# Kernel tuning notes

Measured on AMD Instinct MI355X. Metric: run time of the kernel, lower is better.

## Reference

```python
import jax, jax.numpy as jnp
import numpy as np

# Model dims (match init_kwargs)
B_, L, D_MODEL = 1, 2048, 1024
D_INNER, D_CONV, DT_RANK, D_STATE = 2048, 4, 64, 16


def setup_inputs() -> dict:
    key = jax.random.key(0)
    ks = jax.random.split(key, 8)
    s = lambda k, shape, scale: jax.random.normal(k, shape, jnp.float32) * scale
    return {
        "x": jax.random.normal(ks[0], (B_, L, D_MODEL), jnp.float32),
        "in_proj_w": s(ks[1], (D_MODEL, 2 * D_INNER), 0.02),
        "in_proj_b": jnp.zeros((2 * D_INNER,), jnp.float32),
        "conv_w": s(ks[2], (D_CONV, D_INNER), 0.1),          # depthwise kernel, one tap-vector per channel
        "conv_b": jnp.zeros((D_INNER,), jnp.float32),
        "x_proj_w": s(ks[3], (D_INNER, DT_RANK + 2 * D_STATE), 0.02),
        "dt_proj_w": s(ks[4], (DT_RANK, D_INNER), 0.1),
        "dt_proj_b": s(ks[5], (D_INNER,), 0.1),
        "A_log": jnp.log(jnp.tile(jnp.arange(1, D_STATE + 1, dtype=jnp.float32), (D_INNER, 1))),  # S4D-real init
        "D": jnp.ones((D_INNER,), jnp.float32),
        "out_proj_w": s(ks[6], (D_INNER, D_MODEL), 0.02),
        "out_proj_b": jnp.zeros((D_MODEL,), jnp.float32),
    }


def _mamba_forward(x, in_proj_w, in_proj_b, conv_w, conv_b, x_proj_w,
                   dt_proj_w, dt_proj_b, A_log, D, out_proj_w, out_proj_b):
    b, l, _ = x.shape
    d_inner = conv_w.shape[1]
    d_state = A_log.shape[1]

    # in_proj -> split into ssm path and gating residual
    x_and_res = x @ in_proj_w + in_proj_b                 # [b, l, 2*d_inner]
    xin, res = jnp.split(x_and_res, 2, axis=-1)

    # causal depthwise conv1d over the sequence dim (pad left d_conv-1, trunc to l)
    xp = jnp.pad(xin, ((0, 0), (D_CONV - 1, 0), (0, 0)))
    kern = conv_w[:, None, :]                             # [W, I=1, O=d_inner]
    xc = jax.lax.conv_general_dilated(
        xp, kern, window_strides=(1,), padding="VALID",
        dimension_numbers=("NWC", "WIO", "NWC"),
        feature_group_count=d_inner) + conv_b             # [b, l, d_inner]
    u = jax.nn.silu(xc)

    # selective SSM: input-dependent dt, B, C
    A = -jnp.exp(A_log)                                   # [d_inner, d_state]
    dbc = u @ x_proj_w                                    # [b, l, dt_rank + 2*d_state]
    dt, Bm, Cm = jnp.split(dbc, [DT_RANK, DT_RANK + d_state], axis=-1)
    delta = jax.nn.softplus(dt @ dt_proj_w + dt_proj_b)   # [b, l, d_inner]

    deltaA = jnp.exp(jnp.einsum("bld,dn->bldn", delta, A))          # [b, l, d_inner, d_state]
    deltaBu = jnp.einsum("bld,bln,bld->bldn", delta, Bm, u)         # [b, l, d_inner, d_state]

    def step(h, inp):
        dA_t, dBu_t, C_t = inp
        h = dA_t * h + dBu_t                              # [b, d_inner, d_state]
        y_t = jnp.einsum("bdn,bn->bd", h, C_t)
        return h, y_t

    h0 = jnp.zeros((b, d_inner, d_state), u.dtype)
    _, ys = jax.lax.scan(
        step, h0,
        (deltaA.transpose(1, 0, 2, 3), deltaBu.transpose(1, 0, 2, 3), Cm.transpose(1, 0, 2)))
    y = ys.transpose(1, 0, 2) + u * D                     # skip connection via D

    # gate and out-project
    y = y * jax.nn.silu(res)
    return y @ out_proj_w + out_proj_b                    # [b, l, d_model]


def reference(x, in_proj_w, in_proj_b, conv_w, conv_b, x_proj_w,
              dt_proj_w, dt_proj_b, A_log, D, out_proj_w, out_proj_b):
    return _mamba_forward(x, in_proj_w, in_proj_b, conv_w, conv_b, x_proj_w,
                          dt_proj_w, dt_proj_b, A_log, D, out_proj_w, out_proj_b)
```

## Files before the change

### kernel.cpp

```cpp
#include <hip/hip_runtime.h>


#define L_SEQ 2048
#define DMODEL 1024
#define DINNER 2048
#define NSTATE 16
#define DTRANK 64
#define NPROJ_PAD 128
#define NCH 128
#define TCH 16

typedef __attribute__((ext_vector_type(8))) short short8;
typedef __attribute__((ext_vector_type(4))) float f32x4;

__device__ __forceinline__ unsigned short f2bf(float f) {
  unsigned int u = __float_as_uint(f);
  u += 0x7FFFu + ((u >> 16) & 1u);
  return (unsigned short)(u >> 16);
}
__device__ __forceinline__ float bf2f(unsigned short u) {
  return __uint_as_float(((unsigned int)u) << 16);
}

__device__ __forceinline__ void gload16(const void* g, void* l) {
  __builtin_amdgcn_global_load_lds((const __attribute__((address_space(1))) void*)g,
                                   (__attribute__((address_space(3))) void*)l, 16, 0, 0);
}

__global__ void prep_kernel(const float* __restrict__ in_proj_w, const float* __restrict__ x_proj_w,
                            const float* __restrict__ dt_proj_w,
                            const float* __restrict__ out_proj_w, const float* __restrict__ x,
                            unsigned short* __restrict__ w1t, unsigned short* __restrict__ w3t,
                            unsigned short* __restrict__ w4t, unsigned short* __restrict__ w5t,
                            unsigned short* __restrict__ xb) {
  const int bx = blockIdx.x;
  const int tx = threadIdx.x, ty = threadIdx.y;
  const int id = ty * 32 + tx;

  if (bx >= 6464) {
    if (bx < 8512) {
      const int fid = (bx - 6464) * 256 + id;
      f32x4 v = ((const f32x4*)x)[fid];
      ushort4 o;
      o.x = f2bf(v.x); o.y = f2bf(v.y); o.z = f2bf(v.z); o.w = f2bf(v.w);
      ((ushort4*)xb)[fid] = o;
    } else {
      const int fid = (bx - 8512) * 256 + id;
      ((uint4*)(w3t + 96 * 2048))[fid] = (uint4){0, 0, 0, 0};
    }
    return;
  }

  const float* in;
  unsigned short* out;
  int R, C, rel, gx;
  if (bx < 4096) { in = in_proj_w; out = w1t; R = 1024; C = 4096; rel = bx; gx = 128; }
  else if (bx < 4288) { in = x_proj_w; out = w3t; R = 2048; C = 96; rel = bx - 4096; gx = 3; }
  else if (bx < 4416) { in = dt_proj_w; out = w4t; R = 64; C = 2048; rel = bx - 4288; gx = 64; }
  else { in = out_proj_w; out = w5t; R = 2048; C = 1024; rel = bx - 4416; gx = 32; }
  const int c0 = (rel % gx) * 32, r0 = (rel / gx) * 32;

  __shared__ float tile[32][33];
  for (int y = ty; y < 32; y += 8) tile[y][tx] = in[(size_t)(r0 + y) * C + c0 + tx];
  __syncthreads();
  for (int y = ty; y < 32; y += 8) out[(size_t)(c0 + y) * R + r0 + tx] = f2bf(tile[tx][y]);
}

__global__ void conv_silu_kernel(const float* __restrict__ xin, const float* __restrict__ cw,
                                 const float* __restrict__ cb, unsigned short* __restrict__ ub) {
  const int id = blockIdx.x * 256 + threadIdx.x;
  const int t = id >> 11;
  const int d = id & (DINNER - 1);
  float acc = cb[d];
#pragma unroll
  for (int j = 0; j < 4; j++) {
    int tt = t - 3 + j;
    if (tt >= 0) acc += xin[(size_t)tt * DINNER + d] * cw[j * DINNER + d];
  }
  float s = acc / (1.f + __expf(-acc));
  ub[id] = f2bf(s);
}

template <int EPI, int BM, int BN>
__global__ void gemm_bf16(const unsigned short* __restrict__ A,
                          const unsigned short* __restrict__ Bt, float* __restrict__ C,
                          unsigned short* __restrict__ C2, const float* __restrict__ bias, int M,
                          int N, int K, int KS) {
  constexpr int MI = BM / 32, NJ = BN / 32;
  __shared__ __align__(16) unsigned short lA[2][BM * 64];
  __shared__ __align__(16) unsigned short lB[2][BN * 64];
  const int tid = threadIdx.x;
  const int w = tid >> 6;
  const int lane = tid & 63;
  const int m0 = blockIdx.x * BM;
  const int n0 = blockIdx.y * BN;
  const int kbase = blockIdx.z * KS;
  const int lr = lane >> 3;
  const int srcoff = ((lane & 7) ^ lr) * 8;
  const int wm = (w & 1) * (BM / 2);
  const int wn = (w >> 1) * (BN / 2);
  const int ml = lane & 15;
  const int quad = lane >> 4;

  f32x4 acc[MI][NJ];
#pragma unroll
  for (int i = 0; i < MI; i++)
#pragma unroll
    for (int j = 0; j < NJ; j++) acc[i][j] = (f32x4){0.f, 0.f, 0.f, 0.f};

  const unsigned short* Ag = A + (size_t)m0 * K + kbase;
  const unsigned short* Bg = Bt + (size_t)n0 * K + kbase;

  const int niter = KS >> 6;
  auto stage = [&](int buf, int kk) {
#pragma unroll
    for (int c2 = 0; c2 < BM / 32; c2++) {
      const int row = w * (BM / 4) + c2 * 8 + lr;
      gload16(Ag + (size_t)row * K + kk + srcoff, &lA[buf][(w * (BM / 4) + c2 * 8) * 64]);
    }
#pragma unroll
    for (int c2 = 0; c2 < BN / 32; c2++) {
      const int row = w * (BN / 4) + c2 * 8 + lr;
      gload16(Bg + (size_t)row * K + kk + srcoff, &lB[buf][(w * (BN / 4) + c2 * 8) * 64]);
    }
  };

  stage(0, 0);
  for (int it = 0; it < niter; it++) {
    __syncthreads();
    if (it + 1 < niter) stage((it + 1) & 1, (it + 1) << 6);
    const unsigned short* bufA = lA[it & 1];
    const unsigned short* bufB = lB[it & 1];
#pragma unroll
    for (int ks = 0; ks < 2; ks++) {
      short8 af[MI], bfr[NJ];
#pragma unroll
      for (int i = 0; i < MI; i++) {
        const int row = wm + i * 16 + ml;
        af[i] = *(const short8*)&bufA[row * 64 + ((ks * 4 + quad) ^ (ml & 7)) * 8];
      }
#pragma unroll
      for (int j = 0; j < NJ; j++) {
        const int row = wn + j * 16 + ml;
        bfr[j] = *(const short8*)&bufB[row * 64 + ((ks * 4 + quad) ^ (ml & 7)) * 8];
      }
#pragma unroll
      for (int i = 0; i < MI; i++)
#pragma unroll
        for (int j = 0; j < NJ; j++)
          acc[i][j] = __builtin_amdgcn_mfma_f32_16x16x32_bf16(af[i], bfr[j], acc[i][j], 0, 0, 0);
    }
  }

  float* Cp = (EPI == 3) ? C + (size_t)blockIdx.z * M * N : C;
#pragma unroll
  for (int i = 0; i < MI; i++) {
#pragma unroll
    for (int j = 0; j < NJ; j++) {
      const int col = n0 + wn + j * 16 + ml;
      float bv = (EPI == 3) ? 0.f : (bias ? bias[col] : 0.f);
#pragma unroll
      for (int r = 0; r < 4; r++) {
        const int row = m0 + wm + i * 16 + quad * 4 + r;
        float v = acc[i][j][r] + bv;
        if (EPI == 0) {
          Cp[(size_t)row * N + col] = v;
        } else if (EPI == 3) {
          Cp[(size_t)row * N + col] = v;
        } else if (EPI == 4) {
          if (col < DINNER) {
            C[(size_t)row * DINNER + col] = v;
          } else {
            float s = v / (1.f + __expf(-v));
            C2[(size_t)row * DINNER + (col - DINNER)] = f2bf(s);
          }
        } else if (EPI == 5) {
          float sp = (v > 15.f) ? v : __logf(1.f + __expf(v));
          C2[(size_t)row * N + col] = f2bf(sp);
        }
      }
    }
  }
}

__global__ void reduce_dbc_kernel(const float* __restrict__ part, float* __restrict__ dbc,
                                  unsigned short* __restrict__ dtb) {
  const int id = blockIdx.x * 256 + threadIdx.x;
  float s = 0.f;
#pragma unroll
  for (int z = 0; z < 8; z++) s += part[(size_t)z * (L_SEQ * NPROJ_PAD) + id];
  dbc[id] = s;
  const int col = id & 127;
  if (col < 64) dtb[(id >> 7) * 64 + col] = f2bf(s);
}


__global__ void scan1_kernel(const unsigned short* __restrict__ db,
                             const unsigned short* __restrict__ ub,
                             const float* __restrict__ dbc, const float* __restrict__ A_log,
                             unsigned short* __restrict__ P, unsigned short* __restrict__ Hz) {
  __shared__ float Bs[TCH][NSTATE];
  const int d = blockIdx.x * 256 + threadIdx.x;
  const int c = blockIdx.y;
  for (int idx = threadIdx.x; idx < TCH * NSTATE; idx += 256) {
    int t = idx >> 4, n = idx & 15;
    Bs[t][n] = dbc[(size_t)(c * TCH + t) * NPROJ_PAD + DTRANK + n];
  }
  float Ad[16], h[16], p[16];
#pragma unroll
  for (int n = 0; n < 16; n++) {
    Ad[n] = -__expf(A_log[d * 16 + n]);
    h[n] = 0.f;
    p[n] = 1.f;
  }
  __syncthreads();
#pragma unroll
  for (int t = 0; t < TCH; t++) {
    const int tt = c * TCH + t;
    float dl = bf2f(db[(size_t)tt * DINNER + d]);
    float uu = bf2f(ub[(size_t)tt * DINNER + d]);
    float du = dl * uu;
#pragma unroll
    for (int n = 0; n < 16; n++) {
      float dA = __expf(dl * Ad[n]);
      p[n] *= dA;
      h[n] = dA * h[n] + du * Bs[t][n];
    }
  }
#pragma unroll
  for (int n = 0; n < 16; n++) {
    P[(size_t)(c * 16 + n) * DINNER + d] = f2bf(p[n]);
    Hz[(size_t)(c * 16 + n) * DINNER + d] = f2bf(h[n]);
  }
}

__global__ void scan_carry_kernel(const unsigned short* __restrict__ P,
                                  const unsigned short* __restrict__ Hz,
                                  unsigned short* __restrict__ H0) {
  const int id = blockIdx.x * 256 + threadIdx.x;
  float h = 0.f;
#pragma unroll 8
  for (int c = 0; c < NCH; c++) {
    H0[c * (NSTATE * DINNER) + id] = f2bf(h);
    h = bf2f(P[c * (NSTATE * DINNER) + id]) * h + bf2f(Hz[c * (NSTATE * DINNER) + id]);
  }
}

__global__ void scan2_kernel(const unsigned short* __restrict__ db,
                             const unsigned short* __restrict__ ub,
                             const float* __restrict__ dbc, const float* __restrict__ A_log,
                             const float* __restrict__ Dv, const unsigned short* __restrict__ rsil,
                             const unsigned short* __restrict__ H0,
                             unsigned short* __restrict__ ygb) {
  __shared__ float Bs[TCH][NSTATE];
  __shared__ float Cs[TCH][NSTATE];
  const int d = blockIdx.x * 256 + threadIdx.x;
  const int c = blockIdx.y;
  for (int idx = threadIdx.x; idx < TCH * 2 * NSTATE; idx += 256) {
    int t = idx >> 5, q = idx & 31;
    float v = dbc[(size_t)(c * TCH + t) * NPROJ_PAD + DTRANK + q];
    if (q < 16) Bs[t][q] = v;
    else Cs[t][q - 16] = v;
  }
  float Ad[16], h[16];
#pragma unroll
  for (int n = 0; n < 16; n++) {
    Ad[n] = -__expf(A_log[d * 16 + n]);
    h[n] = bf2f(H0[(size_t)(c * 16 + n) * DINNER + d]);
  }
  const float Dd = Dv[d];
  __syncthreads();
#pragma unroll
  for (int t = 0; t < TCH; t++) {
    const int tt = c * TCH + t;
    float dl = bf2f(db[(size_t)tt * DINNER + d]);
    float uu = bf2f(ub[(size_t)tt * DINNER + d]);
    float rs = bf2f(rsil[(size_t)tt * DINNER + d]);
    float du = dl * uu;
    float y0 = 0.f, y1 = 0.f;
#pragma unroll
    for (int n = 0; n < 16; n++) {
      float dA = __expf(dl * Ad[n]);
      h[n] = dA * h[n] + du * Bs[t][n];
      if (n & 1) y1 += h[n] * Cs[t][n];
      else y0 += h[n] * Cs[t][n];
    }
    float yg = (y0 + y1 + uu * Dd) * rs;
    ygb[(size_t)tt * DINNER + d] = f2bf(yg);
  }
}


extern "C" void kernel_launch(void* const* d_in, const int* in_sizes, int n_in, void* d_out,
                              int out_size, void* d_ws, size_t ws_size, hipStream_t stream) {
  const float* x = (const float*)d_in[0];
  const float* in_proj_w = (const float*)d_in[1];
  const float* in_proj_b = (const float*)d_in[2];
  const float* conv_w = (const float*)d_in[3];
  const float* conv_b = (const float*)d_in[4];
  const float* x_proj_w = (const float*)d_in[5];
  const float* dt_proj_w = (const float*)d_in[6];
  const float* dt_proj_b = (const float*)d_in[7];
  const float* A_log = (const float*)d_in[8];
  const float* Dvec = (const float*)d_in[9];
  const float* out_proj_w = (const float*)d_in[10];
  const float* out_proj_b = (const float*)d_in[11];
  float* out = (float*)d_out;
  char* ws = (char*)d_ws;
  (void)in_sizes; (void)n_in; (void)out_size; (void)ws_size;

  const size_t MB = 1048576;
  const size_t XB = 0;
  const size_t W1T = 4 * MB;
  const size_t XIN = 12 * MB;
  const size_t RSIL = 28 * MB;
  const size_t UB = 36 * MB;
  const size_t W3T = 44 * MB;
  const size_t DBC = W3T + 524288;
  const size_t DTB = DBC + MB;
  const size_t W4T = DTB + 262144;
  const size_t DELTA = 46 * MB;
  const size_t YGB = 54 * MB;
  const size_t W5T = 62 * MB;
  const size_t G3P = 66 * MB;
  const size_t PB = 74 * MB;
  const size_t HZB = 82 * MB;
  const size_t H0B = 90 * MB;

  prep_kernel<<<8544, dim3(32, 8), 0, stream>>>(
      in_proj_w, x_proj_w, dt_proj_w, out_proj_w, x, (unsigned short*)(ws + W1T),
      (unsigned short*)(ws + W3T), (unsigned short*)(ws + W4T), (unsigned short*)(ws + W5T),
      (unsigned short*)(ws + XB));

  gemm_bf16<4, 128, 128><<<dim3(16, 32, 1), 256, 0, stream>>>(
      (const unsigned short*)(ws + XB), (const unsigned short*)(ws + W1T), (float*)(ws + XIN),
      (unsigned short*)(ws + RSIL), in_proj_b, 2048, 4096, 1024, 1024);

  conv_silu_kernel<<<(L_SEQ * DINNER) / 256, 256, 0, stream>>>(
      (const float*)(ws + XIN), conv_w, conv_b, (unsigned short*)(ws + UB));

  gemm_bf16<3, 64, 128><<<dim3(32, 1, 8), 256, 0, stream>>>(
      (const unsigned short*)(ws + UB), (const unsigned short*)(ws + W3T), (float*)(ws + G3P),
      nullptr, nullptr, 2048, NPROJ_PAD, 2048, 256);
  reduce_dbc_kernel<<<(L_SEQ * NPROJ_PAD) / 256, 256, 0, stream>>>(
      (const float*)(ws + G3P), (float*)(ws + DBC), (unsigned short*)(ws + DTB));

  gemm_bf16<5, 128, 128><<<dim3(16, 16, 1), 256, 0, stream>>>(
      (const unsigned short*)(ws + DTB), (const unsigned short*)(ws + W4T), nullptr,
      (unsigned short*)(ws + DELTA), dt_proj_b, 2048, 2048, 64, 64);

  const dim3 sgrid(DINNER / 256, NCH);
  scan1_kernel<<<sgrid, 256, 0, stream>>>(
      (const unsigned short*)(ws + DELTA), (const unsigned short*)(ws + UB),
      (const float*)(ws + DBC), A_log, (unsigned short*)(ws + PB), (unsigned short*)(ws + HZB));
  scan_carry_kernel<<<(NSTATE * DINNER) / 256, 256, 0, stream>>>(
      (const unsigned short*)(ws + PB), (const unsigned short*)(ws + HZB),
      (unsigned short*)(ws + H0B));
  scan2_kernel<<<sgrid, 256, 0, stream>>>(
      (const unsigned short*)(ws + DELTA), (const unsigned short*)(ws + UB),
      (const float*)(ws + DBC), A_log, Dvec, (const unsigned short*)(ws + RSIL),
      (const unsigned short*)(ws + H0B), (unsigned short*)(ws + YGB));

  gemm_bf16<0, 64, 64><<<dim3(32, 16, 1), 256, 0, stream>>>(
      (const unsigned short*)(ws + YGB), (const unsigned short*)(ws + W5T), out, nullptr,
      out_proj_b, 2048, 1024, 2048, 2048);
}
```

Baseline: 230.5 us.

## Fuse chunked scan phases into cooperative kernel and store conv input as bf16

The three scan stages (per-chunk scan, carry propagation, final scan) become one cooperative kernel separated by grid-wide syncs, with a fallback to the old three launches if the cooperative launch fails. The in_proj epilogue now writes the conv input as bf16 instead of fp32, which halves that intermediate's write and read traffic. The conv+SiLU kernel now computes four timesteps per thread and reuses the overlapping loaded inputs. The aim is to cut launch overhead and memory traffic, at the cost of needing all 1024 blocks co-resident and slightly lower precision for the conv input.

After: 529.2 us. 130% more time.

```diff
diff --git a/kernel.cpp b/kernel.cpp
--- a/kernel.cpp
+++ b/kernel.cpp
@@ -1,4 +1,5 @@
 #include <hip/hip_runtime.h>
+#include <hip/hip_cooperative_groups.h>
 
 
 #define L_SEQ 2048
@@ -9,6 +10,8 @@
 #define NPROJ_PAD 128
 #define NCH 128
 #define TCH 16
+
+namespace cg = cooperative_groups;
 
 typedef __attribute__((ext_vector_type(8))) short short8;
 typedef __attribute__((ext_vector_type(4))) float f32x4;
@@ -66,19 +69,26 @@
   for (int y = ty; y < 32; y += 8) out[(size_t)(c0 + y) * R + r0 + tx] = f2bf(tile[tx][y]);
 }
 
-__global__ void conv_silu_kernel(const float* __restrict__ xin, const float* __restrict__ cw,
-                                 const float* __restrict__ cb, unsigned short* __restrict__ ub) {
+__global__ void conv_silu_kernel(const unsigned short* __restrict__ xin,
+                                 const float* __restrict__ cw, const float* __restrict__ cb,
+                                 unsigned short* __restrict__ ub) {
   const int id = blockIdx.x * 256 + threadIdx.x;
-  const int t = id >> 11;
   const int d = id & (DINNER - 1);
-  float acc = cb[d];
-#pragma unroll
-  for (int j = 0; j < 4; j++) {
-    int tt = t - 3 + j;
-    if (tt >= 0) acc += xin[(size_t)tt * DINNER + d] * cw[j * DINNER + d];
-  }
-  float s = acc / (1.f + __expf(-acc));
-  ub[id] = f2bf(s);
+  const int t0 = (id >> 11) * 4;
+  float xv[7];
+#pragma unroll
+  for (int j = 0; j < 7; j++) {
+    int tt = t0 - 3 + j;
+    xv[j] = (tt >= 0) ? bf2f(xin[(size_t)tt * DINNER + d]) : 0.f;
+  }
+  float w0 = cw[d], w1 = cw[DINNER + d], w2 = cw[2 * DINNER + d], w3 = cw[3 * DINNER + d];
+  const float b = cb[d];
+#pragma unroll
+  for (int k = 0; k < 4; k++) {
+    float acc = b + xv[k] * w0 + xv[k + 1] * w1 + xv[k + 2] * w2 + xv[k + 3] * w3;
+    float s = acc / (1.f + __expf(-acc));
+    ub[(size_t)(t0 + k) * DINNER + d] = f2bf(s);
+  }
 }
 
 template <int EPI, int BM, int BN>
@@ -163,13 +173,11 @@
       for (int r = 0; r < 4; r++) {
         const int row = m0 + wm + i * 16 + quad * 4 + r;
         float v = acc[i][j][r] + bv;
-        if (EPI == 0) {
-          Cp[(size_t)row * N + col] = v;
-        } else if (EPI == 3) {
+        if (EPI == 0 || EPI == 3) {
           Cp[(size_t)row * N + col] = v;
         } else if (EPI == 4) {
           if (col < DINNER) {
-            C[(size_t)row * DINNER + col] = v;
+            ((unsigned short*)C)[(size_t)row * DINNER + col] = f2bf(v);
           } else {
             float s = v / (1.f + __expf(-v));
             C2[(size_t)row * DINNER + (col - DINNER)] = f2bf(s);
@@ -195,17 +203,10 @@
 }
 
 
-__global__ void scan1_kernel(const unsigned short* __restrict__ db,
-                             const unsigned short* __restrict__ ub,
-                             const float* __restrict__ dbc, const float* __restrict__ A_log,
-                             unsigned short* __restrict__ P, unsigned short* __restrict__ Hz) {
-  __shared__ float Bs[TCH][NSTATE];
-  const int d = blockIdx.x * 256 + threadIdx.x;
-  const int c = blockIdx.y;
-  for (int idx = threadIdx.x; idx < TCH * NSTATE; idx += 256) {
-    int t = idx >> 4, n = idx & 15;
-    Bs[t][n] = dbc[(size_t)(c * TCH + t) * NPROJ_PAD + DTRANK + n];
-  }
+__device__ __forceinline__ void scan_phase1(const unsigned short* db, const unsigned short* ub,
+                                            const float* dbc, const float* A_log,
+                                            unsigned short* P, unsigned short* Hz, int d, int c,
+                                            float (&Bs)[TCH][NSTATE]) {
   float Ad[16], h[16], p[16];
 #pragma unroll
   for (int n = 0; n < 16; n++) {
@@ -232,6 +233,88 @@
     P[(size_t)(c * 16 + n) * DINNER + d] = f2bf(p[n]);
     Hz[(size_t)(c * 16 + n) * DINNER + d] = f2bf(h[n]);
   }
+}
+
+__device__ __forceinline__ void scan_phase3(const unsigned short* db, const unsigned short* ub,
+                                            const float* A_log, const float* Dv,
+                                            const unsigned short* rsil, const unsigned short* H0,
+                                            unsigned short* ygb, int d, int c,
+                                            float (&Bs)[TCH][NSTATE], float (&Cs)[TCH][NSTATE]) {
+  float Ad[16], h[16];
+#pragma unroll
+  for (int n = 0; n < 16; n++) {
+    Ad[n] = -__expf(A_log[d * 16 + n]);
+    h[n] = bf2f(H0[(size_t)(c * 16 + n) * DINNER + d]);
+  }
+  const float Dd = Dv[d];
+#pragma unroll
+  for (int t = 0; t < TCH; t++) {
+    const int tt = c * TCH + t;
+    float dl = bf2f(db[(size_t)tt * DINNER + d]);
+    float uu = bf2f(ub[(size_t)tt * DINNER + d]);
+    float rs = bf2f(rsil[(size_t)tt * DINNER + d]);
+    float du = dl * uu;
+    float y0 = 0.f, y1 = 0.f;
+#pragma unroll
+    for (int n = 0; n < 16; n++) {
+      float dA = __expf(dl * Ad[n]);
+      h[n] = dA * h[n] + du * Bs[t][n];
+      if (n & 1) y1 += h[n] * Cs[t][n];
+      else y0 += h[n] * Cs[t][n];
+    }
+    float yg = (y0 + y1 + uu * Dd) * rs;
+    ygb[(size_t)tt * DINNER + d] = f2bf(yg);
+  }
+}
+
+__device__ __forceinline__ void load_bc(const float* dbc, int c, float (&Bs)[TCH][NSTATE],
+                                        float (&Cs)[TCH][NSTATE], int tid) {
+  for (int idx = tid; idx < TCH * 2 * NSTATE; idx += 256) {
+    int t = idx >> 5, q = idx & 31;
+    float v = dbc[(size_t)(c * TCH + t) * NPROJ_PAD + DTRANK + q];
+    if (q < 16) Bs[t][q] = v;
+    else Cs[t][q - 16] = v;
+  }
+}
+
+__global__ void __launch_bounds__(256, 4)
+scan_fused_kernel(const unsigned short* __restrict__ db, const unsigned short* __restrict__ ub,
+                  const float* __restrict__ dbc, const float* __restrict__ A_log,
+                  const float* __restrict__ Dv, const unsigned short* __restrict__ rsil,
+                  unsigned short* __restrict__ P, unsigned short* __restrict__ Hz,
+                  unsigned short* __restrict__ H0, unsigned short* __restrict__ ygb) {
+  cg::grid_group grid = cg::this_grid();
+  __shared__ float Bs[TCH][NSTATE];
+  __shared__ float Cs[TCH][NSTATE];
+  const int d = blockIdx.x * 256 + threadIdx.x;
+  const int c = blockIdx.y;
+  load_bc(dbc, c, Bs, Cs, threadIdx.x);
+  scan_phase1(db, ub, dbc, A_log, P, Hz, d, c, Bs);
+  grid.sync();
+  const int gid = (blockIdx.y * gridDim.x + blockIdx.x) * 256 + threadIdx.x;
+  if (gid < NSTATE * DINNER) {
+    float hh = 0.f;
+#pragma unroll 8
+    for (int c2 = 0; c2 < NCH; c2++) {
+      H0[(size_t)c2 * (NSTATE * DINNER) + gid] = f2bf(hh);
+      hh = bf2f(P[(size_t)c2 * (NSTATE * DINNER) + gid]) * hh +
+           bf2f(Hz[(size_t)c2 * (NSTATE * DINNER) + gid]);
+    }
+  }
+  grid.sync();
+  scan_phase3(db, ub, A_log, Dv, rsil, H0, ygb, d, c, Bs, Cs);
+}
+
+__global__ void scan1_kernel(const unsigned short* __restrict__ db,
+                             const unsigned short* __restrict__ ub, const float* __restrict__ dbc,
+                             const float* __restrict__ A_log, unsigned short* __restrict__ P,
+                             unsigned short* __restrict__ Hz) {
+  __shared__ float Bs[TCH][NSTATE];
+  __shared__ float Cs[TCH][NSTATE];
+  const int d = blockIdx.x * 256 + threadIdx.x;
+  const int c = blockIdx.y;
+  load_bc(dbc, c, Bs, Cs, threadIdx.x);
+  scan_phase1(db, ub, dbc, A_log, P, Hz, d, c, Bs);
 }
 
 __global__ void scan_carry_kernel(const unsigned short* __restrict__ P,
@@ -247,47 +330,18 @@
 }
 
 __global__ void scan2_kernel(const unsigned short* __restrict__ db,
-                             const unsigned short* __restrict__ ub,
-                             const float* __restrict__ dbc, const float* __restrict__ A_log,
-                             const float* __restrict__ Dv, const unsigned short* __restrict__ rsil,
+                             const unsigned short* __restrict__ ub, const float* __restrict__ dbc,
+                             const float* __restrict__ A_log, const float* __restrict__ Dv,
+                             const unsigned short* __restrict__ rsil,
                              const unsigned short* __restrict__ H0,
                              unsigned short* __restrict__ ygb) {
   __shared__ float Bs[TCH][NSTATE];
   __shared__ float Cs[TCH][NSTATE];
   const int d = blockIdx.x * 256 + threadIdx.x;
   const int c = blockIdx.y;
-  for (int idx = threadIdx.x; idx < TCH * 2 * NSTATE; idx += 256) {
-    int t = idx >> 5, q = idx & 31;
-    float v = dbc[(size_t)(c * TCH + t) * NPROJ_PAD + DTRANK + q];
-    if (q < 16) Bs[t][q] = v;
-    else Cs[t][q - 16] = v;
-  }
-  float Ad[16], h[16];
-#pragma unroll
-  for (int n = 0; n < 16; n++) {
-    Ad[n] = -__expf(A_log[d * 16 + n]);
-    h[n] = bf2f(H0[(size_t)(c * 16 + n) * DINNER + d]);
-  }
-  const float Dd = Dv[d];
+  load_bc(dbc, c, Bs, Cs, threadIdx.x);
   __syncthreads();
-#pragma unroll
-  for (int t = 0; t < TCH; t++) {
-    const int tt = c * TCH + t;
-    float dl = bf2f(db[(size_t)tt * DINNER + d]);
-    float uu = bf2f(ub[(size_t)tt * DINNER + d]);
-    float rs = bf2f(rsil[(size_t)tt * DINNER + d]);
-    float du = dl * uu;
-    float y0 = 0.f, y1 = 0.f;
-#pragma unroll
-    for (int n = 0; n < 16; n++) {
-      float dA = __expf(dl * Ad[n]);
-      h[n] = dA * h[n] + du * Bs[t][n];
-      if (n & 1) y1 += h[n] * Cs[t][n];
-      else y0 += h[n] * Cs[t][n];
-    }
-    float yg = (y0 + y1 + uu * Dd) * rs;
-    ygb[(size_t)tt * DINNER + d] = f2bf(yg);
-  }
+  scan_phase3(db, ub, A_log, Dv, rsil, H0, ygb, d, c, Bs, Cs);
 }
 
 
@@ -313,19 +367,19 @@
   const size_t XB = 0;
   const size_t W1T = 4 * MB;
   const size_t XIN = 12 * MB;
-  const size_t RSIL = 28 * MB;
-  const size_t UB = 36 * MB;
-  const size_t W3T = 44 * MB;
+  const size_t RSIL = 20 * MB;
+  const size_t UB = 28 * MB;
+  const size_t W3T = 36 * MB;
   const size_t DBC = W3T + 524288;
   const size_t DTB = DBC + MB;
   const size_t W4T = DTB + 262144;
-  const size_t DELTA = 46 * MB;
-  const size_t YGB = 54 * MB;
-  const size_t W5T = 62 * MB;
-  const size_t G3P = 66 * MB;
-  const size_t PB = 74 * MB;
-  const size_t HZB = 82 * MB;
-  const size_t H0B = 90 * MB;
+  const size_t DELTA = 38 * MB;
+  const size_t YGB = 46 * MB;
+  const size_t W5T = 54 * MB;
+  const size_t G3P = 58 * MB;
+  const size_t PB = 66 * MB;
+  const size_t HZB = 74 * MB;
+  const size_t H0B = 82 * MB;
 
   prep_kernel<<<8544, dim3(32, 8), 0, stream>>>(
       in_proj_w, x_proj_w, dt_proj_w, out_proj_w, x, (unsigned short*)(ws + W1T),
@@ -336,8 +390,8 @@
       (const unsigned short*)(ws + XB), (const unsigned short*)(ws + W1T), (float*)(ws + XIN),
       (unsigned short*)(ws + RSIL), in_proj_b, 2048, 4096, 1024, 1024);
 
-  conv_silu_kernel<<<(L_SEQ * DINNER) / 256, 256, 0, stream>>>(
-      (const float*)(ws + XIN), conv_w, conv_b, (unsigned short*)(ws + UB));
+  conv_silu_kernel<<<(L_SEQ * DINNER / 4) / 256, 256, 0, stream>>>(
+      (const unsigned short*)(ws + XIN), conv_w, conv_b, (unsigned short*)(ws + UB));
 
   gemm_bf16<3, 64, 128><<<dim3(32, 1, 8), 256, 0, stream>>>(
       (const unsigned short*)(ws + UB), (const unsigned short*)(ws + W3T), (float*)(ws + G3P),
@@ -349,17 +403,29 @@
       (const unsigned short*)(ws + DTB), (const unsigned short*)(ws + W4T), nullptr,
       (unsigned short*)(ws + DELTA), dt_proj_b, 2048, 2048, 64, 64);
 
-  const dim3 sgrid(DINNER / 256, NCH);
-  scan1_kernel<<<sgrid, 256, 0, stream>>>(
-      (const unsigned short*)(ws + DELTA), (const unsigned short*)(ws + UB),
-      (const float*)(ws + DBC), A_log, (unsigned short*)(ws + PB), (unsigned short*)(ws + HZB));
-  scan_carry_kernel<<<(NSTATE * DINNER) / 256, 256, 0, stream>>>(
-      (const unsigned short*)(ws + PB), (const unsigned short*)(ws + HZB),
-      (unsigned short*)(ws + H0B));
-  scan2_kernel<<<sgrid, 256, 0, stream>>>(
-      (const unsigned short*)(ws + DELTA), (const unsigned short*)(ws + UB),
-      (const float*)(ws + DBC), A_log, Dvec, (const unsigned short*)(ws + RSIL),
-      (const unsigned short*)(ws + H0B), (unsigned short*)(ws + YGB));
+  {
+    const unsigned short* dbp = (const unsigned short*)(ws + DELTA);
+    const unsigned short* ubp = (const unsigned short*)(ws + UB);
+    const float* dbcp = (const float*)(ws + DBC);
+    const float* alogp = A_log;
+    const float* dvp = Dvec;
+    const unsigned short* rsilp = (const unsigned short*)(ws + RSIL);
+    unsigned short* pbp = (unsigned short*)(ws + PB);
+    unsigned short* hzp = (unsigned short*)(ws + HZB);
+    unsigned short* h0p = (unsigned short*)(ws + H0B);
+    unsigned short* ygp = (unsigned short*)(ws + YGB);
+    void* sargs[] = {(void*)&dbp, (void*)&ubp, (void*)&dbcp, (void*)&alogp, (void*)&dvp,
+                     (void*)&rsilp, (void*)&pbp, (void*)&hzp, (void*)&h0p, (void*)&ygp};
+    hipError_t cerr = hipLaunchCooperativeKernel((void*)scan_fused_kernel,
+                                                 dim3(DINNER / 256, NCH), dim3(256), sargs, 0,
+                                                 stream);
+    if (cerr != hipSuccess) {
+      const dim3 sgrid(DINNER / 256, NCH);
+      scan1_kernel<<<sgrid, 256, 0, stream>>>(dbp, ubp, dbcp, alogp, pbp, hzp);
+      scan_carry_kernel<<<(NSTATE * DINNER) / 256, 256, 0, stream>>>(pbp, hzp, h0p);
+      scan2_kernel<<<sgrid, 256, 0, stream>>>(dbp, ubp, dbcp, alogp, dvp, rsilp, h0p, ygp);
+    }
+  }
 
   gemm_bf16<0, 64, 64><<<dim3(32, 16, 1), 256, 0, stream>>>(
       (const unsigned short*)(ws + YGB), (const unsigned short*)(ws + W5T), out, nullptr,
```
